# Kernel optimization log

Measured on AMD Instinct MI355X. Metric: run time of the kernel, lower is better.

The kernel has to match this reference:

```python
import jax, jax.numpy as jnp
import numpy as np

LANDMARKS = 80
POINT_LANDMARKS = tuple(range(468, 538))  # 70 hand-region indices
AVG_SET = [[0,40],[40,40],[80,60],[140,60],[200,60],[260,60],[320,50],[370,50],[420,60],[480,63]]
STAT_CAP = 168


def nan_mean(x, axis=0):
    m = jnp.isnan(x)
    num = jnp.where(m, 0.0, x).sum(axis)
    den = jnp.where(m, 0.0, 1.0).sum(axis)
    return num / den


def nan_std(x, axis=0):
    d = x - nan_mean(x, axis=axis)
    return jnp.sqrt(nan_mean(d * d, axis=axis))


def flatten_means_and_stds(x, reshape1):
    # x: [t, L, C] -> stats over frames -> [2L, C] -> (1, reshape1*2)
    out = jnp.concatenate([nan_mean(x, 0), nan_std(x, 0)], axis=0)
    if out.shape[0] > STAT_CAP:
        out = out[:STAT_CAP, :]
    out = out.reshape(1, reshape1 * 2)
    return jnp.where(jnp.isfinite(out), out, jnp.zeros_like(out))


def setup_inputs() -> dict:
    key = jax.random.key(0)
    T, N, C = 32768, 543, 3
    x_in = jax.random.normal(key, (T, N, C), dtype=jnp.float32)
    return {
        "x_in": x_in,
        "num_frames": 16384,
        "segments": 4,
        "input_shape": (16384, 240),
    }


def reference(x_in, num_frames, segments, input_shape):
    # 1) cluster means + point gather -> x: [T, LANDMARKS, 3]
    parts = [jnp.mean(x_in[:, s:s + l, :], axis=1, keepdims=True) for s, l in AVG_SET]
    parts.append(x_in[:, jnp.array(POINT_LANDMARKS), :])
    x = jnp.concatenate(parts, axis=1)

    # 2) symmetric padding loop (axis 1), gated on T % segments as in the original
    xp = x
    rem = x.shape[0] % segments  # shapes are static -> Python int
    for i in range(segments):
        p0 = 1 if (rem > 0 and i % 2 != 0) else 0
        p1 = 1 if (rem > 0 and i % 2 == 0) else 0
        if p0 or p1:
            xp = jnp.pad(xp, ((0, 0), (p0, p1), (0, 0)), mode='symmetric')

    # 3) per-segment nan mean/std stats
    segs = np.array_split(np.arange(xp.shape[0]), segments)
    feats = [flatten_means_and_stds(xp[idx[0]:idx[-1] + 1], input_shape[1]) for idx in segs]
    feats.append(flatten_means_and_stds(x, input_shape[1]))

    # 4) bilinear resize (align_corners=False semantics, no antialias)
    xi = jnp.transpose(x, (2, 0, 1))[None]            # [1, 3, T, L]
    xi = jax.image.resize(xi, (1, 3, num_frames, LANDMARKS), method='bilinear', antialias=False)
    xi = jnp.transpose(xi[0], (1, 2, 0))              # [num_frames, L, 3]
    xi = xi.reshape(1, input_shape[0] * input_shape[1])
    xi = jnp.where(jnp.isnan(xi), jnp.zeros_like(xi), xi)
    feats.append(xi)

    return jnp.concatenate(feats, axis=1)
```

## Files before the change

### kernel.cpp

```cpp
#include <hip/hip_runtime.h>
#include <math.h>

#define T_FRAMES   32768
#define FRAME      1629
#define FPB        32
#define NBLOCKS    (T_FRAMES / FPB)
#define OUT_B_OFF  2400
#define SEG_BLOCKS (NBLOCKS / 4)
#define MID_OFF    ((size_t)NBLOCKS * 480)

__constant__ int c_astart[10] = {0, 40, 80, 140, 200, 260, 320, 370, 420, 480};
__constant__ int c_alen[10]   = {40, 40, 60, 60, 60, 60, 50, 50, 60, 63};

__global__ __launch_bounds__(256) void featgen_main(
    const float* __restrict__ xin, float* __restrict__ out, float* __restrict__ part)
{
    __shared__ float rows[4 * FRAME];
    __shared__ float xavg[4 * 32];

    const int t = threadIdx.x;
    const int b = blockIdx.x;
    const float* src = xin + (size_t)b * (FPB * FRAME);

    const int g8 = t >> 3;
    const int j8 = t & 7;
    int a_s = 0, a_n = 0, a_c = 0;
    float a_inv = 0.0f;
    if (g8 < 30) {
        int l = g8 / 3; a_c = g8 - 3 * l;
        a_s = c_astart[l]; a_n = c_alen[l];
        a_inv = 1.0f / (float)a_n;
    }

    float ssum = 0.0f, ssq = 0.0f;

    for (int u = 0; u < 8; ++u) {
        const float4* s4 = (const float4*)(src + u * (4 * FRAME));
        float4* d4 = (float4*)rows;
        #pragma unroll
        for (int i = 0; i < 7; ++i) {
            int idx = t + i * 256;
            if (idx < FRAME) d4[idx] = s4[idx];
        }
        __syncthreads();

        if (g8 < 30) {
            #pragma unroll
            for (int f = 0; f < 4; ++f) {
                const float* row = rows + f * FRAME;
                float s = 0.0f;
                for (int j = j8; j < a_n; j += 8) s += row[(a_s + j) * 3 + a_c];
                s += __shfl_xor(s, 1, 8);
                s += __shfl_xor(s, 2, 8);
                s += __shfl_xor(s, 4, 8);
                if (j8 == 0) xavg[f * 32 + g8] = s * a_inv;
            }
        }
        __syncthreads();

        if (t < 240) {
            float v0, v1, v2, v3;
            if (t < 30) {
                v0 = xavg[t];      v1 = xavg[32 + t];
                v2 = xavg[64 + t]; v3 = xavg[96 + t];
            } else {
                v0 = rows[t + 1374];
                v1 = rows[FRAME + t + 1374];
                v2 = rows[2 * FRAME + t + 1374];
                v3 = rows[3 * FRAME + t + 1374];
            }
            const size_t row0 = (size_t)b * 16 + (size_t)u * 2;
            out[OUT_B_OFF + row0 * 240 + t]       = 0.5f * (v0 + v1);
            out[OUT_B_OFF + (row0 + 1) * 240 + t] = 0.5f * (v2 + v3);
            ssum += v0 + v1 + v2 + v3;
            ssq  += v0 * v0 + v1 * v1 + v2 * v2 + v3 * v3;
        }
        __syncthreads();
    }

    if (t < 240) {
        part[(size_t)b * 480 + t]       = ssum;
        part[(size_t)b * 480 + 240 + t] = ssq;
    }
}

__global__ __launch_bounds__(512) void reduce_parts(
    const float* __restrict__ part, float* __restrict__ mid)
{
    const int f = blockIdx.x >> 2;
    const int c = blockIdx.x & 3;
    const int t = threadIdx.x;
    if (t >= 480) return;
    const int b0 = f * SEG_BLOCKS + c * (SEG_BLOCKS / 4);
    float s = 0.0f;
    #pragma unroll 4
    for (int b = 0; b < SEG_BLOCKS / 4; ++b)
        s += part[(size_t)(b0 + b) * 480 + t];
    mid[(size_t)blockIdx.x * 480 + t] = s;
}

__global__ __launch_bounds__(256) void finalize_stats(
    const float* __restrict__ mid, float* __restrict__ out)
{
    const int f = blockIdx.x;
    const int t = threadIdx.x;
    if (t >= 240) return;
    float s = 0.0f, q = 0.0f, n;
    if (f < 4) {
        #pragma unroll
        for (int c = 0; c < 4; ++c) {
            s += mid[(size_t)(f * 4 + c) * 480 + t];
            q += mid[(size_t)(f * 4 + c) * 480 + 240 + t];
        }
        n = 8192.0f;
    } else {
        #pragma unroll
        for (int m = 0; m < 16; ++m) {
            s += mid[(size_t)m * 480 + t];
            q += mid[(size_t)m * 480 + 240 + t];
        }
        n = 32768.0f;
    }
    float mean = s / n;
    float var  = q / n - mean * mean;
    var = var < 0.0f ? 0.0f : var;
    out[f * 480 + t]       = mean;
    out[f * 480 + 240 + t] = sqrtf(var);
}

extern "C" void kernel_launch(void* const* d_in, const int* in_sizes, int n_in,
                              void* d_out, int out_size, void* d_ws, size_t ws_size,
                              hipStream_t stream) {
    (void)in_sizes; (void)n_in; (void)out_size; (void)ws_size;
    const float* xin = (const float*)d_in[0];
    float* out  = (float*)d_out;
    float* part = (float*)d_ws;
    float* mid  = part + MID_OFF;

    featgen_main<<<NBLOCKS, 256, 0, stream>>>(xin, out, part);
    reduce_parts<<<16, 512, 0, stream>>>(part, mid);
    finalize_stats<<<5, 256, 0, stream>>>(mid, out);
}
```

Before: 311.5 us.

## Double-buffer frame loads with direct global-to-LDS DMA and halve frames per block

Replaces the register-staged global-to-shared copy with global_load_lds async transfers into two LDS buffers. The next 4-frame unit is prefetched while the current one is reduced, with manual vmcnt waits and raw s_barrier instead of __syncthreads. FPB drops from 32 to 16, doubling the block count and the partial-sum buffer that reduce_parts must read. The aim is to hide load latency; the risks are fragile per-wave vmcnt counting and roughly double LDS use per block, which can lower occupancy.

New measurement: 318.6 us. 1.02x slower.

```diff
diff --git a/kernel.cpp b/kernel.cpp
--- a/kernel.cpp
+++ b/kernel.cpp
@@ -3,24 +3,50 @@
 
 #define T_FRAMES   32768
 #define FRAME      1629
-#define FPB        32
+#define FPB        16
 #define NBLOCKS    (T_FRAMES / FPB)
 #define OUT_B_OFF  2400
 #define SEG_BLOCKS (NBLOCKS / 4)
 #define MID_OFF    ((size_t)NBLOCKS * 480)
+#define UNIT_F4    1629
 
 __constant__ int c_astart[10] = {0, 40, 80, 140, 200, 260, 320, 370, 420, 480};
 __constant__ int c_alen[10]   = {40, 40, 60, 60, 60, 60, 50, 50, 60, 63};
 
+__device__ __forceinline__ void dma16(const float4* g, float4* l) {
+    __builtin_amdgcn_global_load_lds(
+        (const __attribute__((address_space(1))) void*)g,
+        (__attribute__((address_space(3))) void*)l,
+        16, 0, 0);
+}
+
+#define WAIT_VM7()  asm volatile("s_waitcnt vmcnt(7) lgkmcnt(0)" ::: "memory")
+#define WAIT_VM6()  asm volatile("s_waitcnt vmcnt(6) lgkmcnt(0)" ::: "memory")
+#define WAIT_VM0()  asm volatile("s_waitcnt vmcnt(0) lgkmcnt(0)" ::: "memory")
+#define WAIT_LGKM() asm volatile("s_waitcnt lgkmcnt(0)" ::: "memory")
+#define BARRIER()   asm volatile("s_barrier" ::: "memory")
+
 __global__ __launch_bounds__(256) void featgen_main(
     const float* __restrict__ xin, float* __restrict__ out, float* __restrict__ part)
 {
-    __shared__ float rows[4 * FRAME];
+    __shared__ float rows[2][4 * FRAME];
     __shared__ float xavg[4 * 32];
 
-    const int t = threadIdx.x;
-    const int b = blockIdx.x;
-    const float* src = xin + (size_t)b * (FPB * FRAME);
+    const int t    = threadIdx.x;
+    const int w    = t >> 6;
+    const int lane = t & 63;
+    const int b    = blockIdx.x;
+    const float4* src4 = (const float4*)(xin + (size_t)b * (FPB * FRAME));
+
+    auto issue = [&](int buf, int u) {
+        const float4* g = src4 + (size_t)u * UNIT_F4;
+        float4* l = (float4*)rows[buf];
+        #pragma unroll
+        for (int i = 0; i < 7; ++i) {
+            int idx = i * 256 + w * 64 + lane;
+            if (idx < UNIT_F4) dma16(g + idx, l + idx);
+        }
+    };
 
     const int g8 = t >> 3;
     const int j8 = t & 7;
@@ -34,20 +60,22 @@
 
     float ssum = 0.0f, ssq = 0.0f;
 
-    for (int u = 0; u < 8; ++u) {
-        const float4* s4 = (const float4*)(src + u * (4 * FRAME));
-        float4* d4 = (float4*)rows;
-        #pragma unroll
-        for (int i = 0; i < 7; ++i) {
-            int idx = t + i * 256;
-            if (idx < FRAME) d4[idx] = s4[idx];
-        }
-        __syncthreads();
+    issue(0, 0);
+
+    for (int u = 0; u < 4; ++u) {
+        const int cur = u & 1;
+        if (u < 3) issue(cur ^ 1, u + 1);
+
+        if (u < 3) { if (w < 2) WAIT_VM7(); else WAIT_VM6(); }
+        else       { WAIT_VM0(); }
+        BARRIER();
+
+        const float* rbase = rows[cur];
 
         if (g8 < 30) {
             #pragma unroll
             for (int f = 0; f < 4; ++f) {
-                const float* row = rows + f * FRAME;
+                const float* row = rbase + f * FRAME;
                 float s = 0.0f;
                 for (int j = j8; j < a_n; j += 8) s += row[(a_s + j) * 3 + a_c];
                 s += __shfl_xor(s, 1, 8);
@@ -56,7 +84,7 @@
                 if (j8 == 0) xavg[f * 32 + g8] = s * a_inv;
             }
         }
-        __syncthreads();
+        WAIT_LGKM(); BARRIER();
 
         if (t < 240) {
             float v0, v1, v2, v3;
@@ -64,18 +92,18 @@
                 v0 = xavg[t];      v1 = xavg[32 + t];
                 v2 = xavg[64 + t]; v3 = xavg[96 + t];
             } else {
-                v0 = rows[t + 1374];
-                v1 = rows[FRAME + t + 1374];
-                v2 = rows[2 * FRAME + t + 1374];
-                v3 = rows[3 * FRAME + t + 1374];
+                v0 = rbase[t + 1374];
+                v1 = rbase[FRAME + t + 1374];
+                v2 = rbase[2 * FRAME + t + 1374];
+                v3 = rbase[3 * FRAME + t + 1374];
             }
-            const size_t row0 = (size_t)b * 16 + (size_t)u * 2;
+            const size_t row0 = (size_t)b * 8 + (size_t)u * 2;
             out[OUT_B_OFF + row0 * 240 + t]       = 0.5f * (v0 + v1);
             out[OUT_B_OFF + (row0 + 1) * 240 + t] = 0.5f * (v2 + v3);
             ssum += v0 + v1 + v2 + v3;
             ssq  += v0 * v0 + v1 * v1 + v2 * v2 + v3 * v3;
         }
-        __syncthreads();
+        WAIT_LGKM(); BARRIER();
     }
 
     if (t < 240) {
```
